# Kernel optimization log

Hardware: AMD Instinct MI355X
Metric: run time of the kernel (lower is better)

The kernel has to match this reference:

```python
import jax, jax.numpy as jnp
import numpy as np

N_ATOMS = 500_000
N_BONDS = 1_000_000
NODE, EDGE, OUT = 128, 64, 128
N_PER_DEG = 125_000
DEGREES = (1, 2, 3, 4)
BN_EPS = 1e-5


def setup_inputs() -> dict:
    key = jax.random.key(0)
    ks = jax.random.split(key, 12)
    inp = {
        "atom_repr": jax.random.normal(ks[0], (N_ATOMS, NODE), dtype=jnp.float32),
        "bond_repr": jax.random.normal(ks[1], (N_BONDS, EDGE), dtype=jnp.float32),
    }
    for i, d in enumerate(DEGREES):
        inp[f"atom_idx_d{d}"] = jax.random.randint(jax.random.fold_in(ks[2], i), (N_PER_DEG, d), 0, N_ATOMS, dtype=jnp.int32)
        inp[f"bond_idx_d{d}"] = jax.random.randint(jax.random.fold_in(ks[3], i), (N_PER_DEG, d), 0, N_BONDS, dtype=jnp.int32)
        inp[f"W_d{d}"] = jax.random.normal(jax.random.fold_in(ks[4], i), (OUT, NODE + EDGE), dtype=jnp.float32) / np.sqrt(NODE + EDGE)
    inp["W_self"] = jax.random.normal(ks[5], (OUT, NODE), dtype=jnp.float32) / np.sqrt(NODE)
    inp["bias"] = jnp.zeros((1, OUT), dtype=jnp.float32)
    return inp


def reference(atom_repr, bond_repr,
              atom_idx_d1, atom_idx_d2, atom_idx_d3, atom_idx_d4,
              bond_idx_d1, bond_idx_d2, bond_idx_d3, bond_idx_d4,
              W_d1, W_d2, W_d3, W_d4, W_self, bias):
    atom_idxs = (atom_idx_d1, atom_idx_d2, atom_idx_d3, atom_idx_d4)
    bond_idxs = (bond_idx_d1, bond_idx_d2, bond_idx_d3, bond_idx_d4)
    Ws = (W_d1, W_d2, W_d3, W_d4)
    acts = []
    for aidx, bidx, W in zip(atom_idxs, bond_idxs, Ws):
        a = atom_repr[aidx].sum(axis=1)      # [n_d, NODE] gather+sum over neighbors
        b = bond_repr[bidx].sum(axis=1)      # [n_d, EDGE]
        stacked = jnp.concatenate([a, b], axis=1)  # [n_d, NODE+EDGE]
        acts.append(stacked @ W.T)           # [n_d, OUT]
    neighbor_repr = jnp.concatenate(acts, axis=0)  # [N_ATOMS, OUT]
    self_repr = atom_repr @ W_self.T               # [N_ATOMS, OUT]
    x = self_repr + neighbor_repr + bias
    # BatchNorm1d(affine=False), training mode: biased batch stats
    mean = jnp.mean(x, axis=0)
    var = jnp.var(x, axis=0)
    x = (x - mean) * jax.lax.rsqrt(var + BN_EPS)
    return jax.nn.relu(x)
```

## Files before the change

### kernel.cpp

```cpp
#include <hip/hip_runtime.h>

#define NODE 128
#define EDGE 64
#define OUTC 128
#define KTOT 320
#define NPD 125000
#define N_ATOMS_C 500000
#define BROWS 32
#define NB 4
#define NBLK 977
#define LDST 328
#define BN_EPS 1e-5f

typedef short bf16x8 __attribute__((ext_vector_type(8)));
typedef float floatx4 __attribute__((ext_vector_type(4)));

__device__ __forceinline__ unsigned short f2bf(float f) {
    unsigned u = __float_as_uint(f);
    u += 0x7fffu + ((u >> 16) & 1u);
    return (unsigned short)(u >> 16);
}
__device__ __forceinline__ unsigned pack2(float a, float b) {
    return (unsigned)f2bf(a) | ((unsigned)f2bf(b) << 16);
}

__global__ __launch_bounds__(256) void pack_weights_kernel(
    const float* __restrict__ w1, const float* __restrict__ w2,
    const float* __restrict__ w3, const float* __restrict__ w4,
    const float* __restrict__ W_self, float* __restrict__ stats,
    unsigned short* __restrict__ Wcat)
{
    if (blockIdx.x == 0 && threadIdx.x < 256) stats[threadIdx.x] = 0.f;
    const int idx = blockIdx.x * 256 + threadIdx.x;
    if (idx >= 4 * OUTC * KTOT) return;
    const int d   = idx / (OUTC * KTOT);
    const int rem = idx % (OUTC * KTOT);
    const int n = rem / KTOT, k = rem % KTOT;
    const float* wd = (d == 0) ? w1 : (d == 1) ? w2 : (d == 2) ? w3 : w4;
    const float v = (k < NODE) ? W_self[n * NODE + k]
                               : wd[n * (NODE + EDGE) + (k - NODE)];
    Wcat[idx] = f2bf(v);
}

__global__ __launch_bounds__(256) void compute_x_kernel(
    const float* __restrict__ atom_repr, const float* __restrict__ bond_repr,
    const int* __restrict__ a1, const int* __restrict__ b1,
    const int* __restrict__ a2, const int* __restrict__ b2,
    const int* __restrict__ a3, const int* __restrict__ b3,
    const int* __restrict__ a4, const int* __restrict__ b4,
    const unsigned short* __restrict__ Wcat, const float* __restrict__ bias,
    float* __restrict__ out, float* __restrict__ stats)
{
    const int seg = blockIdx.y;
    const int deg = seg + 1;
    const int* aidx = (seg == 0) ? a1 : (seg == 1) ? a2 : (seg == 2) ? a3 : a4;
    const int* bidx = (seg == 0) ? b1 : (seg == 1) ? b2 : (seg == 2) ? b3 : b4;

    __shared__ unsigned short s_feat[BROWS][LDST];
    __shared__ float s_sum[OUTC], s_sq[OUTC];

    const int tid = threadIdx.x;
    if (tid < OUTC) { s_sum[tid] = 0.f; s_sq[tid] = 0.f; }

    const int w    = tid >> 6;
    const int lane = tid & 63;
    const int quad = lane >> 4;
    const int lrow = lane & 15;

    bf16x8 breg[2][10];
    {
        const unsigned short* Wc = Wcat + (size_t)seg * OUTC * KTOT;
        #pragma unroll
        for (int nt = 0; nt < 2; ++nt) {
            const int n = w * 32 + nt * 16 + lrow;
            #pragma unroll
            for (int ks = 0; ks < 10; ++ks) {
                const int k0 = quad * 8 + ks * 32;
                breg[nt][ks] = *reinterpret_cast<const bf16x8*>(Wc + n * KTOT + k0);
            }
        }
    }
    float bias_v[2];
    bias_v[0] = bias[w * 32 + lrow];
    bias_v[1] = bias[w * 32 + 16 + lrow];

    float lsum[2] = {0.f, 0.f}, lsq[2] = {0.f, 0.f};

    const int gr = tid >> 3;
    const int gt = tid & 7;

    for (int b = 0; b < NB; ++b) {
        const int base = (blockIdx.x * NB + b) * BROWS;
        if (base >= NPD) break;

        {
            const int r0 = base + gr;
            const bool valid = (r0 < NPD);
            int ai[4], bi[4];
            #pragma unroll
            for (int j = 0; j < 4; ++j) {
                const bool on = valid && (j < deg);
                ai[j] = on ? aidx[r0 * deg + j] : 0;
                bi[j] = on ? bidx[r0 * deg + j] : 0;
            }
            const float4* ar = (const float4*)atom_repr;
            const float4* br = (const float4*)bond_repr;
            const size_t gi = (size_t)(seg * NPD) + (valid ? r0 : 0);

            #pragma unroll
            for (int h = 0; h < 2; ++h) {
                const int k0 = h * 64 + gt * 8;
                float4 s0 = make_float4(0, 0, 0, 0), s1 = make_float4(0, 0, 0, 0);
                if (valid) {
                    s0 = ar[gi * 32 + (k0 >> 2)];
                    s1 = ar[gi * 32 + (k0 >> 2) + 1];
                }
                uint4 p;
                p.x = pack2(s0.x, s0.y); p.y = pack2(s0.z, s0.w);
                p.z = pack2(s1.x, s1.y); p.w = pack2(s1.z, s1.w);
                *reinterpret_cast<uint4*>(&s_feat[gr][k0]) = p;
                float4 u0 = make_float4(0, 0, 0, 0), u1 = make_float4(0, 0, 0, 0);
                #pragma unroll
                for (int j = 0; j < 4; ++j) {
                    if (j < deg && valid) {
                        const float4 v0 = ar[(size_t)ai[j] * 32 + (k0 >> 2)];
                        const float4 v1 = ar[(size_t)ai[j] * 32 + (k0 >> 2) + 1];
                        u0.x += v0.x; u0.y += v0.y; u0.z += v0.z; u0.w += v0.w;
                        u1.x += v1.x; u1.y += v1.y; u1.z += v1.z; u1.w += v1.w;
                    }
                }
                p.x = pack2(u0.x, u0.y); p.y = pack2(u0.z, u0.w);
                p.z = pack2(u1.x, u1.y); p.w = pack2(u1.z, u1.w);
                *reinterpret_cast<uint4*>(&s_feat[gr][NODE + k0]) = p;
            }
            {
                const int k0 = gt * 8;
                float4 u0 = make_float4(0, 0, 0, 0), u1 = make_float4(0, 0, 0, 0);
                #pragma unroll
                for (int j = 0; j < 4; ++j) {
                    if (j < deg && valid) {
                        const float4 v0 = br[(size_t)bi[j] * 16 + (k0 >> 2)];
                        const float4 v1 = br[(size_t)bi[j] * 16 + (k0 >> 2) + 1];
                        u0.x += v0.x; u0.y += v0.y; u0.z += v0.z; u0.w += v0.w;
                        u1.x += v1.x; u1.y += v1.y; u1.z += v1.z; u1.w += v1.w;
                    }
                }
                uint4 p;
                p.x = pack2(u0.x, u0.y); p.y = pack2(u0.z, u0.w);
                p.z = pack2(u1.x, u1.y); p.w = pack2(u1.z, u1.w);
                *reinterpret_cast<uint4*>(&s_feat[gr][2 * NODE + k0]) = p;
            }
        }
        __syncthreads();

        floatx4 acc[2][2];
        #pragma unroll
        for (int mt = 0; mt < 2; ++mt)
            #pragma unroll
            for (int nt = 0; nt < 2; ++nt) {
                acc[mt][nt][0] = bias_v[nt]; acc[mt][nt][1] = bias_v[nt];
                acc[mt][nt][2] = bias_v[nt]; acc[mt][nt][3] = bias_v[nt];
            }
        #pragma unroll
        for (int ks = 0; ks < 10; ++ks) {
            bf16x8 af[2];
            af[0] = *reinterpret_cast<const bf16x8*>(&s_feat[lrow][quad * 8 + ks * 32]);
            af[1] = *reinterpret_cast<const bf16x8*>(&s_feat[16 + lrow][quad * 8 + ks * 32]);
            #pragma unroll
            for (int mt = 0; mt < 2; ++mt)
                #pragma unroll
                for (int nt = 0; nt < 2; ++nt)
                    acc[mt][nt] = __builtin_amdgcn_mfma_f32_16x16x32_bf16(
                        af[mt], breg[nt][ks], acc[mt][nt], 0, 0, 0);
        }

        #pragma unroll
        for (int mt = 0; mt < 2; ++mt) {
            #pragma unroll
            for (int nt = 0; nt < 2; ++nt) {
                const int n = w * 32 + nt * 16 + lrow;
                #pragma unroll
                for (int r = 0; r < 4; ++r) {
                    const int m = mt * 16 + quad * 4 + r;
                    const int row = base + m;
                    if (row < NPD) {
                        const float v = acc[mt][nt][r];
                        out[(size_t)(seg * NPD + row) * OUTC + n] = v;
                        lsum[nt] += v; lsq[nt] += v * v;
                    }
                }
            }
        }
        __syncthreads();
    }

    atomicAdd(&s_sum[w * 32 + lrow], lsum[0]);
    atomicAdd(&s_sq [w * 32 + lrow], lsq[0]);
    atomicAdd(&s_sum[w * 32 + 16 + lrow], lsum[1]);
    atomicAdd(&s_sq [w * 32 + 16 + lrow], lsq[1]);
    __syncthreads();
    if (tid < OUTC) {
        atomicAdd(&stats[tid], s_sum[tid]);
        atomicAdd(&stats[OUTC + tid], s_sq[tid]);
    }
}

__global__ void finalize_stats_kernel(float* stats) {
    const int o = threadIdx.x;
    const float inv_n = 1.0f / (float)N_ATOMS_C;
    const float mean = stats[o] * inv_n;
    const float var  = stats[OUTC + o] * inv_n - mean * mean;
    stats[o] = mean;
    stats[OUTC + o] = rsqrtf(var + BN_EPS);
}

__global__ __launch_bounds__(256) void bn_relu_kernel(float* __restrict__ x,
                                                      const float* __restrict__ stats) {
    const size_t e = (size_t)blockIdx.x * 256 + threadIdx.x;
    const int c4 = (int)(e & 31);
    const float4 m = ((const float4*)stats)[c4];
    const float4 s = ((const float4*)stats)[32 + c4];
    float4 v = ((float4*)x)[e];
    v.x = fmaxf((v.x - m.x) * s.x, 0.f);
    v.y = fmaxf((v.y - m.y) * s.y, 0.f);
    v.z = fmaxf((v.z - m.z) * s.z, 0.f);
    v.w = fmaxf((v.w - m.w) * s.w, 0.f);
    ((float4*)x)[e] = v;
}

extern "C" void kernel_launch(void* const* d_in, const int* in_sizes, int n_in,
                              void* d_out, int out_size, void* d_ws, size_t ws_size,
                              hipStream_t stream) {
    const float* atom_repr = (const float*)d_in[0];
    const float* bond_repr = (const float*)d_in[1];
    const int*   a1 = (const int*)d_in[2];
    const int*   b1 = (const int*)d_in[3];
    const float* w1 = (const float*)d_in[4];
    const int*   a2 = (const int*)d_in[5];
    const int*   b2 = (const int*)d_in[6];
    const float* w2 = (const float*)d_in[7];
    const int*   a3 = (const int*)d_in[8];
    const int*   b3 = (const int*)d_in[9];
    const float* w3 = (const float*)d_in[10];
    const int*   a4 = (const int*)d_in[11];
    const int*   b4 = (const int*)d_in[12];
    const float* w4 = (const float*)d_in[13];
    const float* W_self = (const float*)d_in[14];
    const float* bias   = (const float*)d_in[15];

    float* out   = (float*)d_out;
    float* stats = (float*)d_ws;
    unsigned short* Wcat = (unsigned short*)((char*)d_ws + 1024);

    pack_weights_kernel<<<(4 * OUTC * KTOT + 255) / 256, 256, 0, stream>>>(
        w1, w2, w3, w4, W_self, stats, Wcat);

    dim3 grid(NBLK, 4);
    compute_x_kernel<<<grid, 256, 0, stream>>>(
        atom_repr, bond_repr, a1, b1, a2, b2, a3, b3, a4, b4,
        Wcat, bias, out, stats);

    finalize_stats_kernel<<<1, 128, 0, stream>>>(stats);

    bn_relu_kernel<<<(N_ATOMS_C * (OUTC / 4)) / 256, 256, 0, stream>>>(out, stats);
}
```

Measured before the change: 909.0 us.

## Software-pipeline neighbor gathers with double-buffered LDS and interleave degree segments

Gathered atom and bond rows for the next 32-row tile are prefetched into registers while the current tile runs its MFMA GEMM. Shared memory is double-buffered so one barrier per tile replaces two. Blocks now interleave degree segments along blockIdx.x, each processes 8 tiles, and launch bounds ask for 2 blocks per CU. The BN/ReLU pass becomes a grid-stride loop over a fixed number of blocks. The price is a large register footprint (about 28 float4 of staging), which could cause spills or lower occupancy.

```diff
diff --git a/kernel.cpp b/kernel.cpp
--- a/kernel.cpp
+++ b/kernel.cpp
@@ -7,8 +7,8 @@
 #define NPD 125000
 #define N_ATOMS_C 500000
 #define BROWS 32
-#define NB 4
-#define NBLK 977
+#define NB 8
+#define NCHUNK 489
 #define LDST 328
 #define BN_EPS 1e-5f
 
@@ -22,6 +22,9 @@
 }
 __device__ __forceinline__ unsigned pack2(float a, float b) {
     return (unsigned)f2bf(a) | ((unsigned)f2bf(b) << 16);
+}
+__device__ __forceinline__ void add4(float4& a, const float4 b) {
+    a.x += b.x; a.y += b.y; a.z += b.z; a.w += b.w;
 }
 
 __global__ __launch_bounds__(256) void pack_weights_kernel(
@@ -42,7 +45,7 @@
     Wcat[idx] = f2bf(v);
 }
 
-__global__ __launch_bounds__(256) void compute_x_kernel(
+__global__ __launch_bounds__(256, 2) void compute_x_kernel(
     const float* __restrict__ atom_repr, const float* __restrict__ bond_repr,
     const int* __restrict__ a1, const int* __restrict__ b1,
     const int* __restrict__ a2, const int* __restrict__ b2,
@@ -51,12 +54,13 @@
     const unsigned short* __restrict__ Wcat, const float* __restrict__ bias,
     float* __restrict__ out, float* __restrict__ stats)
 {
-    const int seg = blockIdx.y;
+    const int seg   = blockIdx.x & 3;
+    const int chunk = blockIdx.x >> 2;
     const int deg = seg + 1;
     const int* aidx = (seg == 0) ? a1 : (seg == 1) ? a2 : (seg == 2) ? a3 : a4;
     const int* bidx = (seg == 0) ? b1 : (seg == 1) ? b2 : (seg == 2) ? b3 : b4;
 
-    __shared__ unsigned short s_feat[BROWS][LDST];
+    __shared__ unsigned short s_feat[2][BROWS][LDST];
     __shared__ float s_sum[OUTC], s_sq[OUTC];
 
     const int tid = threadIdx.x;
@@ -88,71 +92,86 @@
 
     const int gr = tid >> 3;
     const int gt = tid & 7;
+    const float4* ar = (const float4*)atom_repr;
+    const float4* br = (const float4*)bond_repr;
+
+    float4 st_s[4];
+    float4 st_a[16];
+    float4 st_b[8];
+
+    auto issue = [&](int b) {
+        const int r0 = chunk * (BROWS * NB) + b * BROWS + gr;
+        const int rc = (r0 < NPD) ? r0 : 0;
+        const size_t gi = (size_t)(seg * NPD) + rc;
+        int ai[4], bi[4];
+        #pragma unroll
+        for (int j = 0; j < 4; ++j)
+            if (j < deg) { ai[j] = aidx[rc * deg + j]; bi[j] = bidx[rc * deg + j]; }
+        #pragma unroll
+        for (int h = 0; h < 2; ++h) {
+            const int c = h * 16 + gt * 2;
+            st_s[h * 2 + 0] = ar[gi * 32 + c];
+            st_s[h * 2 + 1] = ar[gi * 32 + c + 1];
+            #pragma unroll
+            for (int j = 0; j < 4; ++j)
+                if (j < deg) {
+                    st_a[j * 4 + h * 2 + 0] = ar[(size_t)ai[j] * 32 + c];
+                    st_a[j * 4 + h * 2 + 1] = ar[(size_t)ai[j] * 32 + c + 1];
+                }
+        }
+        const int cb = gt * 2;
+        #pragma unroll
+        for (int j = 0; j < 4; ++j)
+            if (j < deg) {
+                st_b[j * 2 + 0] = br[(size_t)bi[j] * 16 + cb];
+                st_b[j * 2 + 1] = br[(size_t)bi[j] * 16 + cb + 1];
+            }
+    };
+
+    issue(0);
 
     for (int b = 0; b < NB; ++b) {
-        const int base = (blockIdx.x * NB + b) * BROWS;
+        const int base = chunk * (BROWS * NB) + b * BROWS;
         if (base >= NPD) break;
 
         {
-            const int r0 = base + gr;
-            const bool valid = (r0 < NPD);
-            int ai[4], bi[4];
-            #pragma unroll
-            for (int j = 0; j < 4; ++j) {
-                const bool on = valid && (j < deg);
-                ai[j] = on ? aidx[r0 * deg + j] : 0;
-                bi[j] = on ? bidx[r0 * deg + j] : 0;
-            }
-            const float4* ar = (const float4*)atom_repr;
-            const float4* br = (const float4*)bond_repr;
-            const size_t gi = (size_t)(seg * NPD) + (valid ? r0 : 0);
-
+            unsigned short (*sf)[LDST] = s_feat[b & 1];
             #pragma unroll
             for (int h = 0; h < 2; ++h) {
                 const int k0 = h * 64 + gt * 8;
-                float4 s0 = make_float4(0, 0, 0, 0), s1 = make_float4(0, 0, 0, 0);
-                if (valid) {
-                    s0 = ar[gi * 32 + (k0 >> 2)];
-                    s1 = ar[gi * 32 + (k0 >> 2) + 1];
-                }
                 uint4 p;
-                p.x = pack2(s0.x, s0.y); p.y = pack2(s0.z, s0.w);
-                p.z = pack2(s1.x, s1.y); p.w = pack2(s1.z, s1.w);
-                *reinterpret_cast<uint4*>(&s_feat[gr][k0]) = p;
-                float4 u0 = make_float4(0, 0, 0, 0), u1 = make_float4(0, 0, 0, 0);
+                p.x = pack2(st_s[h * 2].x, st_s[h * 2].y);
+                p.y = pack2(st_s[h * 2].z, st_s[h * 2].w);
+                p.z = pack2(st_s[h * 2 + 1].x, st_s[h * 2 + 1].y);
+                p.w = pack2(st_s[h * 2 + 1].z, st_s[h * 2 + 1].w);
+                *reinterpret_cast<uint4*>(&sf[gr][k0]) = p;
+                float4 u0 = st_a[h * 2], u1 = st_a[h * 2 + 1];
                 #pragma unroll
-                for (int j = 0; j < 4; ++j) {
-                    if (j < deg && valid) {
-                        const float4 v0 = ar[(size_t)ai[j] * 32 + (k0 >> 2)];
-                        const float4 v1 = ar[(size_t)ai[j] * 32 + (k0 >> 2) + 1];
-                        u0.x += v0.x; u0.y += v0.y; u0.z += v0.z; u0.w += v0.w;
-                        u1.x += v1.x; u1.y += v1.y; u1.z += v1.z; u1.w += v1.w;
-                    }
-                }
+                for (int j = 1; j < 4; ++j)
+                    if (j < deg) { add4(u0, st_a[j * 4 + h * 2]); add4(u1, st_a[j * 4 + h * 2 + 1]); }
                 p.x = pack2(u0.x, u0.y); p.y = pack2(u0.z, u0.w);
                 p.z = pack2(u1.x, u1.y); p.w = pack2(u1.z, u1.w);
-                *reinterpret_cast<uint4*>(&s_feat[gr][NODE + k0]) = p;
+                *reinterpret_cast<uint4*>(&sf[gr][NODE + k0]) = p;
             }
             {
                 const int k0 = gt * 8;
-                float4 u0 = make_float4(0, 0, 0, 0), u1 = make_float4(0, 0, 0, 0);
+                float4 u0 = st_b[0], u1 = st_b[1];
                 #pragma unroll
-                for (int j = 0; j < 4; ++j) {
-                    if (j < deg && valid) {
-                        const float4 v0 = br[(size_t)bi[j] * 16 + (k0 >> 2)];
-                        const float4 v1 = br[(size_t)bi[j] * 16 + (k0 >> 2) + 1];
-                        u0.x += v0.x; u0.y += v0.y; u0.z += v0.z; u0.w += v0.w;
-                        u1.x += v1.x; u1.y += v1.y; u1.z += v1.z; u1.w += v1.w;
-                    }
-                }
+                for (int j = 1; j < 4; ++j)
+                    if (j < deg) { add4(u0, st_b[j * 2]); add4(u1, st_b[j * 2 + 1]); }
                 uint4 p;
                 p.x = pack2(u0.x, u0.y); p.y = pack2(u0.z, u0.w);
                 p.z = pack2(u1.x, u1.y); p.w = pack2(u1.z, u1.w);
-                *reinterpret_cast<uint4*>(&s_feat[gr][2 * NODE + k0]) = p;
-            }
-        }
-        __syncthreads();
-
+                *reinterpret_cast<uint4*>(&sf[gr][2 * NODE + k0]) = p;
+            }
+        }
+
+        if (b + 1 < NB) issue(b + 1);
+
+        asm volatile("s_waitcnt lgkmcnt(0)" ::: "memory");
+        __builtin_amdgcn_s_barrier();
+
+        unsigned short (*sfr)[LDST] = s_feat[b & 1];
         floatx4 acc[2][2];
         #pragma unroll
         for (int mt = 0; mt < 2; ++mt)
@@ -163,15 +182,12 @@
             }
         #pragma unroll
         for (int ks = 0; ks < 10; ++ks) {
-            bf16x8 af[2];
-            af[0] = *reinterpret_cast<const bf16x8*>(&s_feat[lrow][quad * 8 + ks * 32]);
-            af[1] = *reinterpret_cast<const bf16x8*>(&s_feat[16 + lrow][quad * 8 + ks * 32]);
-            #pragma unroll
-            for (int mt = 0; mt < 2; ++mt)
-                #pragma unroll
-                for (int nt = 0; nt < 2; ++nt)
-                    acc[mt][nt] = __builtin_amdgcn_mfma_f32_16x16x32_bf16(
-                        af[mt], breg[nt][ks], acc[mt][nt], 0, 0, 0);
+            bf16x8 af0 = *reinterpret_cast<const bf16x8*>(&sfr[lrow][quad * 8 + ks * 32]);
+            bf16x8 af1 = *reinterpret_cast<const bf16x8*>(&sfr[16 + lrow][quad * 8 + ks * 32]);
+            acc[0][0] = __builtin_amdgcn_mfma_f32_16x16x32_bf16(af0, breg[0][ks], acc[0][0], 0, 0, 0);
+            acc[0][1] = __builtin_amdgcn_mfma_f32_16x16x32_bf16(af0, breg[1][ks], acc[0][1], 0, 0, 0);
+            acc[1][0] = __builtin_amdgcn_mfma_f32_16x16x32_bf16(af1, breg[0][ks], acc[1][0], 0, 0, 0);
+            acc[1][1] = __builtin_amdgcn_mfma_f32_16x16x32_bf16(af1, breg[1][ks], acc[1][1], 0, 0, 0);
         }
 
         #pragma unroll
@@ -191,7 +207,6 @@
                 }
             }
         }
-        __syncthreads();
     }
 
     atomicAdd(&s_sum[w * 32 + lrow], lsum[0]);
@@ -214,18 +229,24 @@
     stats[OUTC + o] = rsqrtf(var + BN_EPS);
 }
 
+#define BN_TOT (N_ATOMS_C * (OUTC / 4))
+#define BN_BLOCKS 2048
+
 __global__ __launch_bounds__(256) void bn_relu_kernel(float* __restrict__ x,
                                                       const float* __restrict__ stats) {
-    const size_t e = (size_t)blockIdx.x * 256 + threadIdx.x;
-    const int c4 = (int)(e & 31);
+    const int gid = blockIdx.x * 256 + threadIdx.x;
+    const int c4 = gid & 31;
     const float4 m = ((const float4*)stats)[c4];
     const float4 s = ((const float4*)stats)[32 + c4];
-    float4 v = ((float4*)x)[e];
-    v.x = fmaxf((v.x - m.x) * s.x, 0.f);
-    v.y = fmaxf((v.y - m.y) * s.y, 0.f);
-    v.z = fmaxf((v.z - m.z) * s.z, 0.f);
-    v.w = fmaxf((v.w - m.w) * s.w, 0.f);
-    ((float4*)x)[e] = v;
+    const int stride = BN_BLOCKS * 256;
+    for (size_t e = (size_t)gid; e < (size_t)BN_TOT; e += stride) {
+        float4 v = ((float4*)x)[e];
+        v.x = fmaxf((v.x - m.x) * s.x, 0.f);
+        v.y = fmaxf((v.y - m.y) * s.y, 0.f);
+        v.z = fmaxf((v.z - m.z) * s.z, 0.f);
+        v.w = fmaxf((v.w - m.w) * s.w, 0.f);
+        ((float4*)x)[e] = v;
+    }
 }
 
 extern "C" void kernel_launch(void* const* d_in, const int* in_sizes, int n_in,
@@ -255,12 +276,11 @@
     pack_weights_kernel<<<(4 * OUTC * KTOT + 255) / 256, 256, 0, stream>>>(
         w1, w2, w3, w4, W_self, stats, Wcat);
 
-    dim3 grid(NBLK, 4);
-    compute_x_kernel<<<grid, 256, 0, stream>>>(
+    compute_x_kernel<<<NCHUNK * 4, 256, 0, stream>>>(
         atom_repr, bond_repr, a1, b1, a2, b2, a3, b3, a4, b4,
         Wcat, bias, out, stats);
 
     finalize_stats_kernel<<<1, 128, 0, stream>>>(stats);
 
-    bn_relu_kernel<<<(N_ATOMS_C * (OUTC / 4)) / 256, 256, 0, stream>>>(out, stats);
-}
+    bn_relu_kernel<<<BN_BLOCKS, 256, 0, stream>>>(out, stats);
+}
```

Measured after the change: 834.7 us. 1.09x faster.
